# Kernel tuning notes

Hardware: AMD Instinct MI355X
Metric: run time of the kernel (lower is better)

Reference implementation:

```python
import jax, jax.numpy as jnp
import numpy as np

B, IN, OUT, P, NS = 256, 1024, 512, 1000, 128

def setup_inputs() -> dict:
    key = jax.random.key(0)
    ks = jax.random.split(key, 6)
    return {
        "x": jax.random.normal(ks[0], (B, IN), jnp.float32),
        "noise": jax.random.normal(ks[1], (B, NS, P), jnp.float32),
        "fb_w": jax.random.normal(ks[2], (1, IN), jnp.float32) * (1.0 / np.sqrt(IN)),
        "fb_b": jnp.zeros((1,), jnp.float32),
        "decay_param": jnp.full((1,), 0.1, jnp.float32),
        "conv_w": jax.random.normal(ks[3], (P, P, 3), jnp.float32) * (1.0 / np.sqrt(3 * P)),
        "conv_b": jnp.zeros((P,), jnp.float32),
        "out_w": jax.random.normal(ks[4], (OUT, P), jnp.float32) * (1.0 / np.sqrt(P)),
        "out_b": jnp.zeros((OUT,), jnp.float32),
    }


def reference(x, noise, fb_w, fb_b, decay_param, conv_w, conv_b, out_w, out_b):
    # x: [B, IN]; noise: [B, NS, P] (Brownian increments for the SDE kernel)
    n_steps = noise.shape[1]
    dt = 1.0 / n_steps                       # T = 1.0
    sd = jnp.sqrt(jnp.asarray(dt, x.dtype))
    # per-sample feedback value: sigmoid(feedback_controller(x))
    feedback = jax.nn.sigmoid(x @ fb_w.T + fb_b)            # [B, 1]
    # decay value: sigmoid(decay_controller) * 0.5 (scalar)
    decay = jax.nn.sigmoid(decay_param[0]) * 0.5
    retain = 1.0 - decay * dt
    # Batched Euler-Maruyama Brownian SDE: X_{t+1} = (1 - decay*dt) X_t + feedback*sqrt(dt)*eps_t
    eps = jnp.transpose(noise, (1, 0, 2))                    # [NS, B, P]
    x0 = jnp.zeros((x.shape[0], noise.shape[2]), x.dtype)

    def step(X, e):
        Xn = X * retain + feedback * sd * e
        return Xn, Xn

    _, paths = jax.lax.scan(step, x0, eps)                   # [NS, B, P]
    paths_bct = jnp.transpose(paths, (1, 2, 0))              # [B, P, NS]
    # temporal_aggregator: Conv1d(P, P, kernel=3, padding=1) over time, then mean over time
    agg = jax.lax.conv_general_dilated(
        paths_bct, conv_w, window_strides=(1,), padding=[(1, 1)],
        dimension_numbers=("NCH", "OIH", "NCH"))
    agg = (agg + conv_b[None, :, None]).mean(axis=2)         # [B, P]
    # output_projection: P -> OUT
    return agg @ out_w.T + out_b
```

## Files before the change

kernel.cpp:

```cpp
#include <hip/hip_runtime.h>
#include <hip/hip_bf16.h>

#define B_N   256
#define IN_N  1024
#define OUT_N 512
#define P_N   1000
#define NS_N  128

#define K1P   3072
#define N1P   1024
#define K2P   1024
#define SK    16

typedef __attribute__((ext_vector_type(8))) short short8v;
typedef __attribute__((ext_vector_type(4))) float f32x4;
typedef unsigned short ushort_t;

__device__ __forceinline__ float sigmoid_f(float z) { return 1.0f / (1.0f + __expf(-z)); }

__device__ __forceinline__ void split1(float x, ushort_t& h, ushort_t& l) {
    __hip_bfloat16 hb = __float2bfloat16(x);
    float r = x - __bfloat162float(hb);
    __hip_bfloat16 lb = __float2bfloat16(r);
    h = __bfloat16_as_ushort(hb);
    l = __bfloat16_as_ushort(lb);
}

__device__ __forceinline__ void split8(float4 v0, float4 v1, short8v& h, short8v& l) {
    float vv[8] = {v0.x, v0.y, v0.z, v0.w, v1.x, v1.y, v1.z, v1.w};
    #pragma unroll
    for (int j = 0; j < 8; ++j) {
        ushort_t hh, ll;
        split1(vv[j], hh, ll);
        h[j] = (short)hh;
        l[j] = (short)ll;
    }
}

__global__ __launch_bounds__(256) void sde_fused_kernel(const float* __restrict__ x,
                                                        const float* __restrict__ fb_w,
                                                        const float* __restrict__ fb_b,
                                                        const float* __restrict__ noise,
                                                        const float* __restrict__ decay_param,
                                                        ushort_t* __restrict__ Thi,
                                                        ushort_t* __restrict__ Tlo) {
    int b = blockIdx.x;
    int chunk = blockIdx.y;
    int t = threadIdx.x;

    float4 xv = ((const float4*)(x + (size_t)b * IN_N))[t];
    float4 wv = ((const float4*)fb_w)[t];
    float s = xv.x * wv.x + xv.y * wv.y + xv.z * wv.z + xv.w * wv.w;
    __shared__ float red[256];
    red[t] = s;
    __syncthreads();
    for (int off = 128; off >= 1; off >>= 1) {
        if (t < off) red[t] += red[t + off];
        __syncthreads();
    }
    float fbv = sigmoid_f(red[0] + fb_b[0]);

    float decay = sigmoid_f(decay_param[0]) * 0.5f;
    const float dt = 1.0f / NS_N;
    float retain = 1.0f - decay * dt;
    float inv_omr = 1.0f / (decay * dt);

    int c0 = chunk * 512 + t * 2;
    bool act = (c0 < P_N);
    const float* base = noise + (size_t)b * NS_N * P_N + (act ? c0 : 0);

    float sE0 = 0.f, sE1 = 0.f, L0 = 0.f, L1 = 0.f, F0 = 0.f, F1 = 0.f;
    float rp = 1.0f;
    #pragma unroll 8
    for (int s_ = NS_N - 1; s_ >= 0; --s_) {
        float2 e = *(const float2*)(base + (size_t)s_ * P_N);
        sE0 += e.x; sE1 += e.y;
        L0 += rp * e.x; L1 += rp * e.y;
        if (s_ == 0) { F0 = e.x; F1 = e.y; }
        rp *= retain;
    }

    float sd = sqrtf(dt);
    float scale = act ? (fbv * sd * (1.0f / NS_N)) : 0.0f;
    size_t tb = (size_t)b * K1P + 3 * (size_t)c0;
    float Ls[2] = {L0, L1}, Ss[2] = {sE0, sE1}, Fs[2] = {F0, F1};
    #pragma unroll
    for (int j = 0; j < 2; ++j) {
        float Aj = (Ss[j] - retain * Ls[j]) * inv_omr;
        float t0 = scale * (Aj - Ls[j]);
        float t1 = scale * Aj;
        float t2 = scale * (Aj - Fs[j]);
        ushort_t h, l;
        split1(t0, h, l); Thi[tb + 3 * j + 0] = h; Tlo[tb + 3 * j + 0] = l;
        split1(t1, h, l); Thi[tb + 3 * j + 1] = h; Tlo[tb + 3 * j + 1] = l;
        split1(t2, h, l); Thi[tb + 3 * j + 2] = h; Tlo[tb + 3 * j + 2] = l;
    }
}

__global__ __launch_bounds__(512) void gemm_hilo_mfma(const ushort_t* __restrict__ Ahi,
                                                      const ushort_t* __restrict__ Alo,
                                                      const float* __restrict__ B,
                                                      float* __restrict__ Cpart,
                                                      int lda, int ldb,
                                                      int Nvalid, int Kvalid,
                                                      int Kper, int ldc) {
    __shared__ __align__(16) ushort_t As_hi[128 * 64];
    __shared__ __align__(16) ushort_t As_lo[128 * 64];
    __shared__ __align__(16) ushort_t Bs_hi[128 * 64];
    __shared__ __align__(16) ushort_t Bs_lo[128 * 64];

    const int tid  = threadIdx.x;
    const int lane = tid & 63;
    const int wave = tid >> 6;
    const int r15  = lane & 15;
    const int g4   = lane >> 4;
    const int wrow = wave >> 2;
    const int wcol = wave & 3;
    const int n0 = blockIdx.x * 128;
    const int m0 = blockIdx.y * 128;
    const size_t kbeg = (size_t)blockIdx.z * Kper;

    f32x4 acc[4][2] = {};

    for (int kt = 0; kt < Kper; kt += 64) {
        const size_t kk0 = kbeg + kt;
        #pragma unroll
        for (int c = 0; c < 2; ++c) {
            int chunk = tid + c * 512;
            int row = chunk >> 3;
            int g   = chunk & 7;
            int ldsoff = row * 64 + ((g ^ (row & 7)) << 3);

            const size_t ka = (size_t)(m0 + row) * lda + kk0 + g * 8;
            *(short8v*)&As_hi[ldsoff] = *(const short8v*)(Ahi + ka);
            *(short8v*)&As_lo[ldsoff] = *(const short8v*)(Alo + ka);

            float4 b0 = {0, 0, 0, 0}, b1 = {0, 0, 0, 0};
            if ((n0 + row) < Nvalid && (int)(kk0 + g * 8) < Kvalid) {
                const float* bp = B + (size_t)(n0 + row) * ldb + kk0 + g * 8;
                b0 = *(const float4*)bp;
                b1 = *(const float4*)(bp + 4);
            }
            short8v bh, bl;
            split8(b0, b1, bh, bl);
            *(short8v*)&Bs_hi[ldsoff] = bh;
            *(short8v*)&Bs_lo[ldsoff] = bl;
        }
        __syncthreads();

        #pragma unroll
        for (int ks = 0; ks < 2; ++ks) {
            const int g = ks * 4 + g4;
            short8v ah[4], al[4], bh[2], bl[2];
            #pragma unroll
            for (int f = 0; f < 4; ++f) {
                int arow = wrow * 64 + f * 16 + r15;
                int aoff = arow * 64 + ((g ^ (arow & 7)) << 3);
                ah[f] = *(const short8v*)&As_hi[aoff];
                al[f] = *(const short8v*)&As_lo[aoff];
            }
            #pragma unroll
            for (int f = 0; f < 2; ++f) {
                int brow = wcol * 32 + f * 16 + r15;
                int boff = brow * 64 + ((g ^ (brow & 7)) << 3);
                bh[f] = *(const short8v*)&Bs_hi[boff];
                bl[f] = *(const short8v*)&Bs_lo[boff];
            }
            #pragma unroll
            for (int mf = 0; mf < 4; ++mf) {
                #pragma unroll
                for (int nf = 0; nf < 2; ++nf) {
                    acc[mf][nf] = __builtin_amdgcn_mfma_f32_16x16x32_bf16(ah[mf], bh[nf], acc[mf][nf], 0, 0, 0);
                    acc[mf][nf] = __builtin_amdgcn_mfma_f32_16x16x32_bf16(ah[mf], bl[nf], acc[mf][nf], 0, 0, 0);
                    acc[mf][nf] = __builtin_amdgcn_mfma_f32_16x16x32_bf16(al[mf], bh[nf], acc[mf][nf], 0, 0, 0);
                }
            }
        }
        __syncthreads();
    }

    float* cp = Cpart + (size_t)blockIdx.z * 256 * ldc;
    #pragma unroll
    for (int mf = 0; mf < 4; ++mf) {
        #pragma unroll
        for (int nf = 0; nf < 2; ++nf) {
            #pragma unroll
            for (int r = 0; r < 4; ++r) {
                int m = m0 + wrow * 64 + mf * 16 + g4 * 4 + r;
                int n = n0 + wcol * 32 + nf * 16 + r15;
                cp[(size_t)m * ldc + n] = acc[mf][nf][r];
            }
        }
    }
}

__global__ __launch_bounds__(256) void reduce_agg_kernel(const float* __restrict__ Cpart,
                                                         const float* __restrict__ conv_b,
                                                         ushort_t* __restrict__ agg_hi,
                                                         ushort_t* __restrict__ agg_lo) {
    int idx = blockIdx.x * 256 + threadIdx.x;
    int n = idx & (N1P - 1);
    float s = 0.f;
    if (n < P_N) {
        s = conv_b[n];
        #pragma unroll
        for (int z = 0; z < SK; ++z) s += Cpart[(size_t)z * (B_N * N1P) + idx];
    }
    ushort_t h, l;
    split1(s, h, l);
    agg_hi[idx] = h;
    agg_lo[idx] = l;
}

__global__ __launch_bounds__(256) void reduce_out_kernel(const float* __restrict__ Cpart,
                                                         const float* __restrict__ out_b,
                                                         float* __restrict__ out) {
    int idx = blockIdx.x * 256 + threadIdx.x;
    int n = idx & (OUT_N - 1);
    float s = out_b[n];
    #pragma unroll
    for (int z = 0; z < SK; ++z) s += Cpart[(size_t)z * (B_N * OUT_N) + idx];
    out[idx] = s;
}

extern "C" void kernel_launch(void* const* d_in, const int* in_sizes, int n_in,
                              void* d_out, int out_size, void* d_ws, size_t ws_size,
                              hipStream_t stream) {
    const float* x           = (const float*)d_in[0];
    const float* noise       = (const float*)d_in[1];
    const float* fb_w        = (const float*)d_in[2];
    const float* fb_b        = (const float*)d_in[3];
    const float* decay_param = (const float*)d_in[4];
    const float* conv_w      = (const float*)d_in[5];
    const float* conv_b      = (const float*)d_in[6];
    const float* out_w       = (const float*)d_in[7];
    const float* out_b       = (const float*)d_in[8];
    float* out = (float*)d_out;

    char* ws = (char*)d_ws;
    size_t off = 0;
    ushort_t* Thi   = (ushort_t*)(ws + off); off += (size_t)B_N * K1P * 2;
    ushort_t* Tlo   = (ushort_t*)(ws + off); off += (size_t)B_N * K1P * 2;
    ushort_t* AgHi  = (ushort_t*)(ws + off); off += (size_t)B_N * K2P * 2;
    ushort_t* AgLo  = (ushort_t*)(ws + off); off += (size_t)B_N * K2P * 2;
    float*    Cpart = (float*)(ws + off);    off += (size_t)SK * B_N * N1P * 4;

    {
        dim3 grid(B_N, 2);
        sde_fused_kernel<<<grid, 256, 0, stream>>>(x, fb_w, fb_b, noise, decay_param, Thi, Tlo);
    }

    {
        dim3 grid(N1P / 128, B_N / 128, SK);
        gemm_hilo_mfma<<<grid, 512, 0, stream>>>(Thi, Tlo, conv_w, Cpart,
                                                 K1P, 3 * P_N, P_N, 3 * P_N,
                                                 K1P / SK, N1P);
        reduce_agg_kernel<<<(B_N * N1P) / 256, 256, 0, stream>>>(Cpart, conv_b, AgHi, AgLo);
    }

    {
        dim3 grid(OUT_N / 128, B_N / 128, SK);
        gemm_hilo_mfma<<<grid, 512, 0, stream>>>(AgHi, AgLo, out_w, Cpart,
                                                 K2P, P_N, OUT_N, P_N,
                                                 K2P / SK, OUT_N);
        reduce_out_kernel<<<(B_N * OUT_N) / 256, 256, 0, stream>>>(Cpart, out_b, out);
    }
}
```

Measured before the change: 53.40 us.

## Split SDE time reduction in halves and fuse split-K reduce into second GEMM

The noise scan is split into two time halves computed by separate blocks with float4 loads. A combine kernel merges them using retain^64 and then forms the bf16 hi/lo conv operands. The separate reduce_agg pass is removed: the output GEMM sums the 16 split-K partials and adds the conv bias while loading its A tiles, and its own split-K drops to 8. This removes one launch and one intermediate buffer, at the cost of an extra launch for the combine step and the output GEMM re-reading the partials once per N block.

```diff
diff --git a/kernel.cpp b/kernel.cpp
--- a/kernel.cpp
+++ b/kernel.cpp
@@ -10,7 +10,8 @@
 #define K1P   3072
 #define N1P   1024
 #define K2P   1024
-#define SK    16
+#define SK1   16
+#define SK2   8
 
 typedef __attribute__((ext_vector_type(8))) short short8v;
 typedef __attribute__((ext_vector_type(4))) float f32x4;
@@ -37,16 +38,52 @@
     }
 }
 
-__global__ __launch_bounds__(256) void sde_fused_kernel(const float* __restrict__ x,
-                                                        const float* __restrict__ fb_w,
-                                                        const float* __restrict__ fb_b,
-                                                        const float* __restrict__ noise,
-                                                        const float* __restrict__ decay_param,
-                                                        ushort_t* __restrict__ Thi,
-                                                        ushort_t* __restrict__ Tlo) {
-    int b = blockIdx.x;
-    int chunk = blockIdx.y;
-    int t = threadIdx.x;
+__global__ __launch_bounds__(128) void sde_partial_kernel(const float* __restrict__ noise,
+                                                          const float* __restrict__ decay_param,
+                                                          float* __restrict__ SE,
+                                                          float* __restrict__ LL,
+                                                          float* __restrict__ FF) {
+    const int b  = blockIdx.x;
+    const int ch = blockIdx.y;
+    const int th = blockIdx.z;
+    const int t  = threadIdx.x;
+    const int c0 = ch * 512 + t * 4;
+    if (c0 >= P_N) return;
+
+    float decay = sigmoid_f(decay_param[0]) * 0.5f;
+    const float dt = 1.0f / NS_N;
+    float retain = 1.0f - decay * dt;
+
+    const float* base = noise + (size_t)b * NS_N * P_N + c0;
+    const int s0 = th * 64;
+
+    float4 sE = {0, 0, 0, 0}, L = {0, 0, 0, 0};
+    float rp = 1.0f;
+    #pragma unroll 16
+    for (int s = s0 + 63; s >= s0; --s) {
+        float4 e = *(const float4*)(base + (size_t)s * P_N);
+        sE.x += e.x; sE.y += e.y; sE.z += e.z; sE.w += e.w;
+        L.x += rp * e.x; L.y += rp * e.y; L.z += rp * e.z; L.w += rp * e.w;
+        rp *= retain;
+    }
+
+    size_t o = ((size_t)th * B_N + b) * 1024 + c0;
+    *(float4*)(SE + o) = sE;
+    *(float4*)(LL + o) = L;
+    if (th == 0) *(float4*)(FF + (size_t)b * 1024 + c0) = *(const float4*)base;
+}
+
+__global__ __launch_bounds__(256) void combine_kernel(const float* __restrict__ x,
+                                                      const float* __restrict__ fb_w,
+                                                      const float* __restrict__ fb_b,
+                                                      const float* __restrict__ decay_param,
+                                                      const float* __restrict__ SE,
+                                                      const float* __restrict__ LL,
+                                                      const float* __restrict__ FF,
+                                                      ushort_t* __restrict__ Thi,
+                                                      ushort_t* __restrict__ Tlo) {
+    const int b = blockIdx.x;
+    const int t = threadIdx.x;
 
     float4 xv = ((const float4*)(x + (size_t)b * IN_N))[t];
     float4 wv = ((const float4*)fb_w)[t];
@@ -64,32 +101,38 @@
     const float dt = 1.0f / NS_N;
     float retain = 1.0f - decay * dt;
     float inv_omr = 1.0f / (decay * dt);
-
-    int c0 = chunk * 512 + t * 2;
-    bool act = (c0 < P_N);
-    const float* base = noise + (size_t)b * NS_N * P_N + (act ? c0 : 0);
-
-    float sE0 = 0.f, sE1 = 0.f, L0 = 0.f, L1 = 0.f, F0 = 0.f, F1 = 0.f;
-    float rp = 1.0f;
-    #pragma unroll 8
-    for (int s_ = NS_N - 1; s_ >= 0; --s_) {
-        float2 e = *(const float2*)(base + (size_t)s_ * P_N);
-        sE0 += e.x; sE1 += e.y;
-        L0 += rp * e.x; L1 += rp * e.y;
-        if (s_ == 0) { F0 = e.x; F1 = e.y; }
-        rp *= retain;
-    }
+    float r2 = retain * retain, r4 = r2 * r2, r8 = r4 * r4;
+    float r16 = r8 * r8, r32 = r16 * r16, r64 = r32 * r32;
+
+    const int c0 = t * 4;
+    size_t tb = (size_t)b * K1P + 3 * (size_t)c0;
+    if (c0 >= P_N) {
+        #pragma unroll
+        for (int j = 0; j < 12; ++j) { Thi[tb + j] = 0; Tlo[tb + j] = 0; }
+        return;
+    }
+
+    size_t o0 = ((size_t)0 * B_N + b) * 1024 + c0;
+    size_t o1 = ((size_t)1 * B_N + b) * 1024 + c0;
+    float4 se0 = *(const float4*)(SE + o0);
+    float4 se1 = *(const float4*)(SE + o1);
+    float4 ll0 = *(const float4*)(LL + o0);
+    float4 ll1 = *(const float4*)(LL + o1);
+    float4 ff  = *(const float4*)(FF + (size_t)b * 1024 + c0);
 
     float sd = sqrtf(dt);
-    float scale = act ? (fbv * sd * (1.0f / NS_N)) : 0.0f;
-    size_t tb = (size_t)b * K1P + 3 * (size_t)c0;
-    float Ls[2] = {L0, L1}, Ss[2] = {sE0, sE1}, Fs[2] = {F0, F1};
+    float scale = fbv * sd * (1.0f / NS_N);
+
+    float Se[4] = {se0.x + se1.x, se0.y + se1.y, se0.z + se1.z, se0.w + se1.w};
+    float Lv[4] = {ll1.x + r64 * ll0.x, ll1.y + r64 * ll0.y, ll1.z + r64 * ll0.z, ll1.w + r64 * ll0.w};
+    float Fv[4] = {ff.x, ff.y, ff.z, ff.w};
+
     #pragma unroll
-    for (int j = 0; j < 2; ++j) {
-        float Aj = (Ss[j] - retain * Ls[j]) * inv_omr;
-        float t0 = scale * (Aj - Ls[j]);
+    for (int j = 0; j < 4; ++j) {
+        float Aj = (Se[j] - retain * Lv[j]) * inv_omr;
+        float t0 = scale * (Aj - Lv[j]);
         float t1 = scale * Aj;
-        float t2 = scale * (Aj - Fs[j]);
+        float t2 = scale * (Aj - Fv[j]);
         ushort_t h, l;
         split1(t0, h, l); Thi[tb + 3 * j + 0] = h; Tlo[tb + 3 * j + 0] = l;
         split1(t1, h, l); Thi[tb + 3 * j + 1] = h; Tlo[tb + 3 * j + 1] = l;
@@ -194,32 +237,127 @@
     }
 }
 
-__global__ __launch_bounds__(256) void reduce_agg_kernel(const float* __restrict__ Cpart,
-                                                         const float* __restrict__ conv_b,
-                                                         ushort_t* __restrict__ agg_hi,
-                                                         ushort_t* __restrict__ agg_lo) {
-    int idx = blockIdx.x * 256 + threadIdx.x;
-    int n = idx & (N1P - 1);
-    float s = 0.f;
-    if (n < P_N) {
-        s = conv_b[n];
-        #pragma unroll
-        for (int z = 0; z < SK; ++z) s += Cpart[(size_t)z * (B_N * N1P) + idx];
-    }
-    ushort_t h, l;
-    split1(s, h, l);
-    agg_hi[idx] = h;
-    agg_lo[idx] = l;
-}
-
-__global__ __launch_bounds__(256) void reduce_out_kernel(const float* __restrict__ Cpart,
+__global__ __launch_bounds__(512) void gemm2_fused_kernel(const float* __restrict__ Cpart1,
+                                                          const float* __restrict__ conv_b,
+                                                          const float* __restrict__ out_w,
+                                                          float* __restrict__ Cpart2) {
+    __shared__ __align__(16) ushort_t As_hi[128 * 64];
+    __shared__ __align__(16) ushort_t As_lo[128 * 64];
+    __shared__ __align__(16) ushort_t Bs_hi[128 * 64];
+    __shared__ __align__(16) ushort_t Bs_lo[128 * 64];
+
+    const int tid  = threadIdx.x;
+    const int lane = tid & 63;
+    const int wave = tid >> 6;
+    const int r15  = lane & 15;
+    const int g4   = lane >> 4;
+    const int wrow = wave >> 2;
+    const int wcol = wave & 3;
+    const int n0 = blockIdx.x * 128;
+    const int m0 = blockIdx.y * 128;
+    const int kbeg = blockIdx.z * (K2P / SK2);
+
+    f32x4 acc[4][2] = {};
+
+    for (int kt = 0; kt < K2P / SK2; kt += 64) {
+        const int kk0 = kbeg + kt;
+        #pragma unroll
+        for (int c = 0; c < 2; ++c) {
+            int chunk = tid + c * 512;
+            int row = chunk >> 3;
+            int g   = chunk & 7;
+            int ldsoff = row * 64 + ((g ^ (row & 7)) << 3);
+            int k = kk0 + g * 8;
+
+            float4 a0 = {0, 0, 0, 0}, a1 = {0, 0, 0, 0};
+            {
+                const float* cp = Cpart1 + (size_t)(m0 + row) * N1P + k;
+                #pragma unroll
+                for (int z = 0; z < SK1; ++z) {
+                    float4 p0 = *(const float4*)(cp + (size_t)z * (B_N * N1P));
+                    float4 p1 = *(const float4*)(cp + (size_t)z * (B_N * N1P) + 4);
+                    a0.x += p0.x; a0.y += p0.y; a0.z += p0.z; a0.w += p0.w;
+                    a1.x += p1.x; a1.y += p1.y; a1.z += p1.z; a1.w += p1.w;
+                }
+                if (k < P_N) {
+                    float4 c0v = *(const float4*)(conv_b + k);
+                    float4 c1v = *(const float4*)(conv_b + k + 4);
+                    a0.x += c0v.x; a0.y += c0v.y; a0.z += c0v.z; a0.w += c0v.w;
+                    a1.x += c1v.x; a1.y += c1v.y; a1.z += c1v.z; a1.w += c1v.w;
+                }
+            }
+            short8v ah, al;
+            split8(a0, a1, ah, al);
+            *(short8v*)&As_hi[ldsoff] = ah;
+            *(short8v*)&As_lo[ldsoff] = al;
+
+            float4 b0 = {0, 0, 0, 0}, b1 = {0, 0, 0, 0};
+            if (k < P_N) {
+                const float* bp = out_w + (size_t)(n0 + row) * P_N + k;
+                b0 = *(const float4*)bp;
+                b1 = *(const float4*)(bp + 4);
+            }
+            short8v bh, bl;
+            split8(b0, b1, bh, bl);
+            *(short8v*)&Bs_hi[ldsoff] = bh;
+            *(short8v*)&Bs_lo[ldsoff] = bl;
+        }
+        __syncthreads();
+
+        #pragma unroll
+        for (int ks = 0; ks < 2; ++ks) {
+            const int g = ks * 4 + g4;
+            short8v ah[4], al[4], bh[2], bl[2];
+            #pragma unroll
+            for (int f = 0; f < 4; ++f) {
+                int arow = wrow * 64 + f * 16 + r15;
+                int aoff = arow * 64 + ((g ^ (arow & 7)) << 3);
+                ah[f] = *(const short8v*)&As_hi[aoff];
+                al[f] = *(const short8v*)&As_lo[aoff];
+            }
+            #pragma unroll
+            for (int f = 0; f < 2; ++f) {
+                int brow = wcol * 32 + f * 16 + r15;
+                int boff = brow * 64 + ((g ^ (brow & 7)) << 3);
+                bh[f] = *(const short8v*)&Bs_hi[boff];
+                bl[f] = *(const short8v*)&Bs_lo[boff];
+            }
+            #pragma unroll
+            for (int mf = 0; mf < 4; ++mf) {
+                #pragma unroll
+                for (int nf = 0; nf < 2; ++nf) {
+                    acc[mf][nf] = __builtin_amdgcn_mfma_f32_16x16x32_bf16(ah[mf], bh[nf], acc[mf][nf], 0, 0, 0);
+                    acc[mf][nf] = __builtin_amdgcn_mfma_f32_16x16x32_bf16(ah[mf], bl[nf], acc[mf][nf], 0, 0, 0);
+                    acc[mf][nf] = __builtin_amdgcn_mfma_f32_16x16x32_bf16(al[mf], bh[nf], acc[mf][nf], 0, 0, 0);
+                }
+            }
+        }
+        __syncthreads();
+    }
+
+    float* cp = Cpart2 + (size_t)blockIdx.z * (B_N * OUT_N);
+    #pragma unroll
+    for (int mf = 0; mf < 4; ++mf) {
+        #pragma unroll
+        for (int nf = 0; nf < 2; ++nf) {
+            #pragma unroll
+            for (int r = 0; r < 4; ++r) {
+                int m = m0 + wrow * 64 + mf * 16 + g4 * 4 + r;
+                int n = n0 + wcol * 32 + nf * 16 + r15;
+                cp[(size_t)m * OUT_N + n] = acc[mf][nf][r];
+            }
+        }
+    }
+}
+
+__global__ __launch_bounds__(256) void reduce_out_kernel(const float* __restrict__ Cpart2,
                                                          const float* __restrict__ out_b,
                                                          float* __restrict__ out) {
     int idx = blockIdx.x * 256 + threadIdx.x;
     int n = idx & (OUT_N - 1);
     float s = out_b[n];
     #pragma unroll
-    for (int z = 0; z < SK; ++z) s += Cpart[(size_t)z * (B_N * OUT_N) + idx];
+    for (int z = 0; z < SK2; ++z) s += Cpart2[(size_t)z * (B_N * OUT_N) + idx];
     out[idx] = s;
 }
 
@@ -239,30 +377,32 @@
 
     char* ws = (char*)d_ws;
     size_t off = 0;
-    ushort_t* Thi   = (ushort_t*)(ws + off); off += (size_t)B_N * K1P * 2;
-    ushort_t* Tlo   = (ushort_t*)(ws + off); off += (size_t)B_N * K1P * 2;
-    ushort_t* AgHi  = (ushort_t*)(ws + off); off += (size_t)B_N * K2P * 2;
-    ushort_t* AgLo  = (ushort_t*)(ws + off); off += (size_t)B_N * K2P * 2;
-    float*    Cpart = (float*)(ws + off);    off += (size_t)SK * B_N * N1P * 4;
+    float*    SE     = (float*)(ws + off);    off += (size_t)2 * B_N * 1024 * 4;
+    float*    LL     = (float*)(ws + off);    off += (size_t)2 * B_N * 1024 * 4;
+    float*    FF     = (float*)(ws + off);    off += (size_t)B_N * 1024 * 4;
+    ushort_t* Thi    = (ushort_t*)(ws + off); off += (size_t)B_N * K1P * 2;
+    ushort_t* Tlo    = (ushort_t*)(ws + off); off += (size_t)B_N * K1P * 2;
+    float*    Cpart1 = (float*)(ws + off);    off += (size_t)SK1 * B_N * N1P * 4;
+    float*    Cpart2 = (float*)(ws + off);    off += (size_t)SK2 * B_N * OUT_N * 4;
 
     {
-        dim3 grid(B_N, 2);
-        sde_fused_kernel<<<grid, 256, 0, stream>>>(x, fb_w, fb_b, noise, decay_param, Thi, Tlo);
-    }
+        dim3 grid(B_N, 2, 2);
+        sde_partial_kernel<<<grid, 128, 0, stream>>>(noise, decay_param, SE, LL, FF);
+    }
+
+    combine_kernel<<<B_N, 256, 0, stream>>>(x, fb_w, fb_b, decay_param, SE, LL, FF, Thi, Tlo);
 
     {
-        dim3 grid(N1P / 128, B_N / 128, SK);
-        gemm_hilo_mfma<<<grid, 512, 0, stream>>>(Thi, Tlo, conv_w, Cpart,
+        dim3 grid(N1P / 128, B_N / 128, SK1);
+        gemm_hilo_mfma<<<grid, 512, 0, stream>>>(Thi, Tlo, conv_w, Cpart1,
                                                  K1P, 3 * P_N, P_N, 3 * P_N,
-                                                 K1P / SK, N1P);
-        reduce_agg_kernel<<<(B_N * N1P) / 256, 256, 0, stream>>>(Cpart, conv_b, AgHi, AgLo);
+                                                 K1P / SK1, N1P);
     }
 
     {
-        dim3 grid(OUT_N / 128, B_N / 128, SK);
-        gemm_hilo_mfma<<<grid, 512, 0, stream>>>(AgHi, AgLo, out_w, Cpart,
-                                                 K2P, P_N, OUT_N, P_N,
-                                                 K2P / SK, OUT_N);
-        reduce_out_kernel<<<(B_N * OUT_N) / 256, 256, 0, stream>>>(Cpart, out_b, out);
-    }
-}
+        dim3 grid(OUT_N / 128, B_N / 128, SK2);
+        gemm2_fused_kernel<<<grid, 512, 0, stream>>>(Cpart1, conv_b, out_w, Cpart2);
+    }
+
+    reduce_out_kernel<<<(B_N * OUT_N) / 256, 256, 0, stream>>>(Cpart2, out_b, out);
+}
```

Result: slower. 65.82 us (+23.3%).
